# Kernel tuning notes

Hardware: AMD Instinct MI355X
Metric: run time of the kernel (lower is better)

## Reference

```python
import jax, jax.numpy as jnp
import numpy as np
import math

B, N, F_IN, F_OUT = 16, 2048, 256, 64


def setup_inputs() -> dict:
    key = jax.random.key(0)
    k1, k2, k3, k4 = jax.random.split(key, 4)
    x = jax.random.normal(k1, (B, N, F_IN), dtype=jnp.float32)
    adj = jax.random.randint(k2, (B, N, N), 0, 2, dtype=jnp.int32)
    stdv = 1.0 / math.sqrt(F_OUT)
    weight = jax.random.uniform(k3, (F_IN, F_OUT), dtype=jnp.float32, minval=-stdv, maxval=stdv)
    # weight2 stdv = 1/sqrt(1) = 1.0
    weight2 = jax.random.uniform(k4, (2 * F_OUT, 1), dtype=jnp.float32, minval=-1.0, maxval=1.0)
    return {"x": x, "adj": adj, "weight": weight, "weight2": weight2}


def reference(x, adj, weight, weight2):
    # h[b,n,o] = (x @ weight)  -- shared linear projection
    h = jnp.einsum("bni,io->bno", x, weight)
    Fo = weight.shape[1]
    # Split additive-attention vector: e_ij = relu(h_i . a_src + h_j . a_dst)
    # Mathematically identical to cat([h_i, h_j]) @ weight2 of the original.
    a_src = weight2[:Fo, 0]
    a_dst = weight2[Fo:, 0]
    s_src = jnp.einsum("bno,o->bn", h, a_src)  # [B, N]
    s_dst = jnp.einsum("bno,o->bn", h, a_dst)  # [B, N]
    e = jax.nn.relu(s_src[:, :, None] + s_dst[:, None, :])  # [B, N, N]
    NEG = jnp.float32(-9e15)
    scores = jnp.where(adj > 0, e, NEG)
    attention = jax.nn.softmax(scores, axis=2)  # softmax over neighbors j
    # dropout = 0.0 / eval mode -> identity
    out = jnp.einsum("bij,bjo->bio", attention, h)  # [B, N, F_OUT]
    return out
```

## Files before the change

### kernel.cpp

```cpp
#include <hip/hip_runtime.h>
#include <hip/hip_bf16.h>

#define BB 16
#define NN 2048
#define FIN 256
#define FO 64
#define CH 256
#define HSTR 264

typedef __bf16 bf16x8 __attribute__((ext_vector_type(8)));
typedef float  f32x4  __attribute__((ext_vector_type(4)));
typedef int    i32x4  __attribute__((ext_vector_type(4)));
typedef unsigned int uint;

__global__ __launch_bounds__(256) void k_pack(const int* __restrict__ adj,
                                              unsigned char* __restrict__ mask) {
    size_t t = (size_t)blockIdx.x * 256 + threadIdx.x;
    const i32x4* ap = (const i32x4*)(adj + t * 8);
    i32x4 a0 = __builtin_nontemporal_load(ap);
    i32x4 a1 = __builtin_nontemporal_load(ap + 1);
    unsigned b = (unsigned)(a0.x > 0) | ((unsigned)(a0.y > 0) << 1) |
                 ((unsigned)(a0.z > 0) << 2) | ((unsigned)(a0.w > 0) << 3) |
                 ((unsigned)(a1.x > 0) << 4) | ((unsigned)(a1.y > 0) << 5) |
                 ((unsigned)(a1.z > 0) << 6) | ((unsigned)(a1.w > 0) << 7);
    mask[t] = (unsigned char)b;
}

__global__ __launch_bounds__(256) void k1_gemm(
    const float* __restrict__ x, const float* __restrict__ weight,
    const float* __restrict__ w2,
    __bf16* __restrict__ hT, float* __restrict__ s_src, float* __restrict__ s_dst) {
    __shared__ __bf16 WtL[FO * 264];
    __shared__ float vsL[FIN], vdL[FIN];
    int t = threadIdx.x;
    {
        const float4* wr = (const float4*)(weight + t * FO);
        float a = 0.f, d = 0.f;
#pragma unroll
        for (int c = 0; c < 16; ++c) {
            float4 v = wr[c];
            int o = c * 4;
            WtL[(o + 0) * 264 + t] = (__bf16)v.x;
            WtL[(o + 1) * 264 + t] = (__bf16)v.y;
            WtL[(o + 2) * 264 + t] = (__bf16)v.z;
            WtL[(o + 3) * 264 + t] = (__bf16)v.w;
            a += v.x * w2[o] + v.y * w2[o + 1] + v.z * w2[o + 2] + v.w * w2[o + 3];
            d += v.x * w2[FO + o] + v.y * w2[FO + o + 1] +
                 v.z * w2[FO + o + 2] + v.w * w2[FO + o + 3];
        }
        vsL[t] = a;
        vdL[t] = d;
    }
    __syncthreads();

    int lane = threadIdx.x & 63, w = threadIdx.x >> 6;
    int quad = lane >> 4, m = lane & 15;
    int Rbase = blockIdx.x * 64 + w * 16;
    int R = Rbase + m;
    const float* xr = x + (long)R * FIN;

    f32x4 acc[4] = {};
    float ps = 0.f, pd = 0.f;

#pragma unroll
    for (int k0 = 0; k0 < FIN; k0 += 32) {
        int kb = k0 + quad * 8;
        float4 x0 = *(const float4*)(xr + kb);
        float4 x1 = *(const float4*)(xr + kb + 4);
        float4 u0 = *(const float4*)(vsL + kb);
        float4 u1 = *(const float4*)(vsL + kb + 4);
        float4 t0 = *(const float4*)(vdL + kb);
        float4 t1 = *(const float4*)(vdL + kb + 4);
        ps += x0.x * u0.x + x0.y * u0.y + x0.z * u0.z + x0.w * u0.w +
              x1.x * u1.x + x1.y * u1.y + x1.z * u1.z + x1.w * u1.w;
        pd += x0.x * t0.x + x0.y * t0.y + x0.z * t0.z + x0.w * t0.w +
              x1.x * t1.x + x1.y * t1.y + x1.z * t1.z + x1.w * t1.w;
        bf16x8 bf = {(__bf16)x0.x, (__bf16)x0.y, (__bf16)x0.z, (__bf16)x0.w,
                     (__bf16)x1.x, (__bf16)x1.y, (__bf16)x1.z, (__bf16)x1.w};
#pragma unroll
        for (int ot = 0; ot < 4; ++ot) {
            bf16x8 af = *(const bf16x8*)(WtL + (ot * 16 + m) * 264 + kb);
            acc[ot] = __builtin_amdgcn_mfma_f32_16x16x32_bf16(af, bf, acc[ot], 0, 0, 0);
        }
    }
    ps += __shfl_xor(ps, 16);
    ps += __shfl_xor(ps, 32);
    pd += __shfl_xor(pd, 16);
    pd += __shfl_xor(pd, 32);
    if (quad == 0) {
        s_src[R] = ps;
        s_dst[R] = pd;
    }
    int b = R >> 11;
    int nb = Rbase & (NN - 1);
#pragma unroll
    for (int ot = 0; ot < 4; ++ot) {
#pragma unroll
        for (int r = 0; r < 4; ++r) {
            int o = ot * 16 + quad * 4 + r;
            hT[((long)b * FO + o) * NN + nb + m] = (__bf16)acc[ot][r];
        }
    }
}

__global__ __launch_bounds__(256, 2) void k2_attn(
    const unsigned char* __restrict__ mask, const float* __restrict__ s_src,
    const float* __restrict__ s_dst, const __bf16* __restrict__ hT,
    float* __restrict__ out) {
    __shared__ __bf16 hL[FO * HSTR];
    __shared__ float EL[NN];
    int b = blockIdx.x >> 5;
    int i0 = (blockIdx.x & 31) << 6;
    int lane = threadIdx.x & 63, w = threadIdx.x >> 6;
    int quad = lane >> 4, m = lane & 15;
    int rowbase = i0 + w * 16;
    int row = rowbase + m;

    const float* sd = s_dst + b * NN;
    float mx = -3.0e38f;
    for (int j = lane; j < NN; j += 64) mx = fmaxf(mx, sd[j]);
#pragma unroll
    for (int off = 32; off >= 1; off >>= 1) mx = fmaxf(mx, __shfl_xor(mx, off));
    {
        int j0 = threadIdx.x * 8;
        float4 v0 = *(const float4*)(sd + j0);
        float4 v1 = *(const float4*)(sd + j0 + 4);
        EL[j0 + 0] = __expf(v0.x - mx);
        EL[j0 + 1] = __expf(v0.y - mx);
        EL[j0 + 2] = __expf(v0.z - mx);
        EL[j0 + 3] = __expf(v0.w - mx);
        EL[j0 + 4] = __expf(v1.x - mx);
        EL[j0 + 5] = __expf(v1.y - mx);
        EL[j0 + 6] = __expf(v1.z - mx);
        EL[j0 + 7] = __expf(v1.w - mx);
    }

    float T = s_src[b * NN + row] + mx;
    float cK = __expf(-T);

    int so = threadIdx.x >> 2;
    int sc = (threadIdx.x & 3) * 64;
    const __bf16* hsrc = hT + ((long)b * FO + so) * NN + sc;
    __bf16* hdst = hL + so * HSTR + sc;

    const uint4* mrow = (const uint4*)(mask + ((size_t)(b * NN + row)) * 256);
    int q8 = quad * 8;

    bf16x8 st[8];
    {
        const bf16x8* sp = (const bf16x8*)hsrc;
#pragma unroll
        for (int i = 0; i < 8; ++i) st[i] = sp[i];
    }
    uint4 mv0 = mrow[0], mv1 = mrow[1];

    f32x4 acc[4] = {};
    f32x4 accL = {};
    const bf16x8 ones = {(__bf16)1.f, (__bf16)1.f, (__bf16)1.f, (__bf16)1.f,
                         (__bf16)1.f, (__bf16)1.f, (__bf16)1.f, (__bf16)1.f};

    for (int c = 0; c < NN / CH; ++c) {
        __syncthreads();
        {
            bf16x8* dp = (bf16x8*)hdst;
#pragma unroll
            for (int i = 0; i < 8; ++i) dp[i] = st[i];
        }
        __syncthreads();
        uint mg[8] = {mv0.x, mv0.y, mv0.z, mv0.w, mv1.x, mv1.y, mv1.z, mv1.w};
        if (c < NN / CH - 1) {
            const bf16x8* sp = (const bf16x8*)(hsrc + (c + 1) * CH);
#pragma unroll
            for (int i = 0; i < 8; ++i) st[i] = sp[i];
            mv0 = mrow[(c + 1) * 2];
            mv1 = mrow[(c + 1) * 2 + 1];
        }
#pragma unroll
        for (int u = 0; u < 8; ++u) {
            int ksg = c * 8 + u;
            uint mb = (mg[u] >> q8) & 0xffu;
            const float* ep = EL + ksg * 32 + q8;
            float4 e0 = *(const float4*)ep;
            float4 e1 = *(const float4*)(ep + 4);
            float p0 = (mb & 1u)   ? fmaxf(e0.x, cK) : 0.f;
            float p1 = (mb & 2u)   ? fmaxf(e0.y, cK) : 0.f;
            float p2 = (mb & 4u)   ? fmaxf(e0.z, cK) : 0.f;
            float p3 = (mb & 8u)   ? fmaxf(e0.w, cK) : 0.f;
            float p4 = (mb & 16u)  ? fmaxf(e1.x, cK) : 0.f;
            float p5 = (mb & 32u)  ? fmaxf(e1.y, cK) : 0.f;
            float p6 = (mb & 64u)  ? fmaxf(e1.z, cK) : 0.f;
            float p7 = (mb & 128u) ? fmaxf(e1.w, cK) : 0.f;
            bf16x8 af = {(__bf16)p0, (__bf16)p1, (__bf16)p2, (__bf16)p3,
                         (__bf16)p4, (__bf16)p5, (__bf16)p6, (__bf16)p7};
            accL = __builtin_amdgcn_mfma_f32_16x16x32_bf16(af, ones, accL, 0, 0, 0);
            const __bf16* hb = hL + u * 32 + q8;
#pragma unroll
            for (int ot = 0; ot < 4; ++ot) {
                bf16x8 bf = *(const bf16x8*)(hb + (ot * 16 + m) * HSTR);
                acc[ot] = __builtin_amdgcn_mfma_f32_16x16x32_bf16(af, bf, acc[ot], 0, 0, 0);
            }
        }
    }

    float* outp = out + ((long)b * NN + rowbase) * FO;
#pragma unroll
    for (int r = 0; r < 4; ++r) {
        int orow = quad * 4 + r;
        float inv = 1.0f / accL[r];
#pragma unroll
        for (int ot = 0; ot < 4; ++ot) {
            outp[(long)orow * FO + ot * 16 + m] = acc[ot][r] * inv;
        }
    }
}

extern "C" void kernel_launch(void* const* d_in, const int* in_sizes, int n_in,
                              void* d_out, int out_size, void* d_ws, size_t ws_size,
                              hipStream_t stream) {
    const float* x      = (const float*)d_in[0];
    const int*   adj    = (const int*)d_in[1];
    const float* weight = (const float*)d_in[2];
    const float* w2     = (const float*)d_in[3];
    float* out = (float*)d_out;

    char* ws = (char*)d_ws;
    __bf16* hT   = (__bf16*)ws;
    float* s_src = (float*)(ws + 4194304);
    float* s_dst = (float*)(ws + 4194304 + 131072);
    unsigned char* mask = (unsigned char*)(ws + 4194304 + 262144);

    k_pack<<<32768, 256, 0, stream>>>(adj, mask);
    k1_gemm<<<512, 256, 0, stream>>>(x, weight, w2, hT, s_src, s_dst);
    k2_attn<<<512, 256, 0, stream>>>(mask, s_src, s_dst, hT, out);
}
```

Before: 408.0 us.

## Process two row tiles per wave and double-buffer h chunks in k2_attn

Each wave now computes 32 output rows instead of 16, sharing each shared-memory h fragment and EL load across two MFMA accumulator sets, and the grid halves to 256 blocks. The h staging buffer is double-buffered so only one barrier per chunk is needed. This is meant to cut shared-memory traffic, redundant per-block softmax preprocessing and sync overhead, at the cost of more registers, one block per CU and fewer total waves to hide latency.

```diff
diff --git a/kernel.cpp b/kernel.cpp
--- a/kernel.cpp
+++ b/kernel.cpp
@@ -103,18 +103,19 @@
     }
 }
 
-__global__ __launch_bounds__(256, 2) void k2_attn(
+__global__ __launch_bounds__(256, 1) void k2_attn(
     const unsigned char* __restrict__ mask, const float* __restrict__ s_src,
     const float* __restrict__ s_dst, const __bf16* __restrict__ hT,
     float* __restrict__ out) {
-    __shared__ __bf16 hL[FO * HSTR];
+    __shared__ __bf16 hL[2][FO * HSTR];
     __shared__ float EL[NN];
-    int b = blockIdx.x >> 5;
-    int i0 = (blockIdx.x & 31) << 6;
+    int b = blockIdx.x >> 4;
+    int i0 = (blockIdx.x & 15) << 7;
     int lane = threadIdx.x & 63, w = threadIdx.x >> 6;
     int quad = lane >> 4, m = lane & 15;
-    int rowbase = i0 + w * 16;
-    int row = rowbase + m;
+    int rowbase = i0 + w * 32;
+    int row0 = rowbase + m;
+    int row1 = rowbase + 16 + m;
 
     const float* sd = s_dst + b * NN;
     float mx = -3.0e38f;
@@ -135,15 +136,16 @@
         EL[j0 + 7] = __expf(v1.w - mx);
     }
 
-    float T = s_src[b * NN + row] + mx;
-    float cK = __expf(-T);
+    float cK0 = __expf(-(s_src[b * NN + row0] + mx));
+    float cK1 = __expf(-(s_src[b * NN + row1] + mx));
 
     int so = threadIdx.x >> 2;
     int sc = (threadIdx.x & 3) * 64;
     const __bf16* hsrc = hT + ((long)b * FO + so) * NN + sc;
-    __bf16* hdst = hL + so * HSTR + sc;
-
-    const uint4* mrow = (const uint4*)(mask + ((size_t)(b * NN + row)) * 256);
+    int ldoff = so * HSTR + sc;
+
+    const uint4* mrow0 = (const uint4*)(mask + ((size_t)(b * NN + row0)) * 256);
+    const uint4* mrow1 = (const uint4*)(mask + ((size_t)(b * NN + row1)) * 256);
     int q8 = quad * 8;
 
     bf16x8 st[8];
@@ -152,64 +154,89 @@
 #pragma unroll
         for (int i = 0; i < 8; ++i) st[i] = sp[i];
     }
-    uint4 mv0 = mrow[0], mv1 = mrow[1];
-
-    f32x4 acc[4] = {};
-    f32x4 accL = {};
+    uint4 ma0 = mrow0[0], ma1 = mrow0[1];
+    uint4 mb0 = mrow1[0], mb1 = mrow1[1];
+    {
+        bf16x8* dp = (bf16x8*)(hL[0] + ldoff);
+#pragma unroll
+        for (int i = 0; i < 8; ++i) dp[i] = st[i];
+    }
+    __syncthreads();
+
+    f32x4 acc0[4] = {}, acc1[4] = {};
+    f32x4 accL0 = {}, accL1 = {};
     const bf16x8 ones = {(__bf16)1.f, (__bf16)1.f, (__bf16)1.f, (__bf16)1.f,
                          (__bf16)1.f, (__bf16)1.f, (__bf16)1.f, (__bf16)1.f};
 
+#pragma unroll
     for (int c = 0; c < NN / CH; ++c) {
-        __syncthreads();
-        {
-            bf16x8* dp = (bf16x8*)hdst;
-#pragma unroll
-            for (int i = 0; i < 8; ++i) dp[i] = st[i];
-        }
-        __syncthreads();
-        uint mg[8] = {mv0.x, mv0.y, mv0.z, mv0.w, mv1.x, mv1.y, mv1.z, mv1.w};
+        const __bf16* cur = hL[c & 1];
+        uint mg0[8] = {ma0.x, ma0.y, ma0.z, ma0.w, ma1.x, ma1.y, ma1.z, ma1.w};
+        uint mg1[8] = {mb0.x, mb0.y, mb0.z, mb0.w, mb1.x, mb1.y, mb1.z, mb1.w};
         if (c < NN / CH - 1) {
             const bf16x8* sp = (const bf16x8*)(hsrc + (c + 1) * CH);
 #pragma unroll
             for (int i = 0; i < 8; ++i) st[i] = sp[i];
-            mv0 = mrow[(c + 1) * 2];
-            mv1 = mrow[(c + 1) * 2 + 1];
+            ma0 = mrow0[(c + 1) * 2];
+            ma1 = mrow0[(c + 1) * 2 + 1];
+            mb0 = mrow1[(c + 1) * 2];
+            mb1 = mrow1[(c + 1) * 2 + 1];
         }
 #pragma unroll
         for (int u = 0; u < 8; ++u) {
-            int ksg = c * 8 + u;
-            uint mb = (mg[u] >> q8) & 0xffu;
-            const float* ep = EL + ksg * 32 + q8;
+            uint mA = (mg0[u] >> q8) & 0xffu;
+            uint mB = (mg1[u] >> q8) & 0xffu;
+            const float* ep = EL + (c * 8 + u) * 32 + q8;
             float4 e0 = *(const float4*)ep;
             float4 e1 = *(const float4*)(ep + 4);
-            float p0 = (mb & 1u)   ? fmaxf(e0.x, cK) : 0.f;
-            float p1 = (mb & 2u)   ? fmaxf(e0.y, cK) : 0.f;
-            float p2 = (mb & 4u)   ? fmaxf(e0.z, cK) : 0.f;
-            float p3 = (mb & 8u)   ? fmaxf(e0.w, cK) : 0.f;
-            float p4 = (mb & 16u)  ? fmaxf(e1.x, cK) : 0.f;
-            float p5 = (mb & 32u)  ? fmaxf(e1.y, cK) : 0.f;
-            float p6 = (mb & 64u)  ? fmaxf(e1.z, cK) : 0.f;
-            float p7 = (mb & 128u) ? fmaxf(e1.w, cK) : 0.f;
-            bf16x8 af = {(__bf16)p0, (__bf16)p1, (__bf16)p2, (__bf16)p3,
-                         (__bf16)p4, (__bf16)p5, (__bf16)p6, (__bf16)p7};
-            accL = __builtin_amdgcn_mfma_f32_16x16x32_bf16(af, ones, accL, 0, 0, 0);
-            const __bf16* hb = hL + u * 32 + q8;
+            float a0 = (mA & 1u)   ? fmaxf(e0.x, cK0) : 0.f;
+            float a1 = (mA & 2u)   ? fmaxf(e0.y, cK0) : 0.f;
+            float a2 = (mA & 4u)   ? fmaxf(e0.z, cK0) : 0.f;
+            float a3 = (mA & 8u)   ? fmaxf(e0.w, cK0) : 0.f;
+            float a4 = (mA & 16u)  ? fmaxf(e1.x, cK0) : 0.f;
+            float a5 = (mA & 32u)  ? fmaxf(e1.y, cK0) : 0.f;
+            float a6 = (mA & 64u)  ? fmaxf(e1.z, cK0) : 0.f;
+            float a7 = (mA & 128u) ? fmaxf(e1.w, cK0) : 0.f;
+            float b0 = (mB & 1u)   ? fmaxf(e0.x, cK1) : 0.f;
+            float b1 = (mB & 2u)   ? fmaxf(e0.y, cK1) : 0.f;
+            float b2 = (mB & 4u)   ? fmaxf(e0.z, cK1) : 0.f;
+            float b3 = (mB & 8u)   ? fmaxf(e0.w, cK1) : 0.f;
+            float b4 = (mB & 16u)  ? fmaxf(e1.x, cK1) : 0.f;
+            float b5 = (mB & 32u)  ? fmaxf(e1.y, cK1) : 0.f;
+            float b6 = (mB & 64u)  ? fmaxf(e1.z, cK1) : 0.f;
+            float b7 = (mB & 128u) ? fmaxf(e1.w, cK1) : 0.f;
+            bf16x8 af0 = {(__bf16)a0, (__bf16)a1, (__bf16)a2, (__bf16)a3,
+                          (__bf16)a4, (__bf16)a5, (__bf16)a6, (__bf16)a7};
+            bf16x8 af1 = {(__bf16)b0, (__bf16)b1, (__bf16)b2, (__bf16)b3,
+                          (__bf16)b4, (__bf16)b5, (__bf16)b6, (__bf16)b7};
+            accL0 = __builtin_amdgcn_mfma_f32_16x16x32_bf16(af0, ones, accL0, 0, 0, 0);
+            accL1 = __builtin_amdgcn_mfma_f32_16x16x32_bf16(af1, ones, accL1, 0, 0, 0);
+            const __bf16* hb = cur + u * 32 + q8;
 #pragma unroll
             for (int ot = 0; ot < 4; ++ot) {
                 bf16x8 bf = *(const bf16x8*)(hb + (ot * 16 + m) * HSTR);
-                acc[ot] = __builtin_amdgcn_mfma_f32_16x16x32_bf16(af, bf, acc[ot], 0, 0, 0);
+                acc0[ot] = __builtin_amdgcn_mfma_f32_16x16x32_bf16(af0, bf, acc0[ot], 0, 0, 0);
+                acc1[ot] = __builtin_amdgcn_mfma_f32_16x16x32_bf16(af1, bf, acc1[ot], 0, 0, 0);
             }
         }
+        if (c < NN / CH - 1) {
+            bf16x8* dp = (bf16x8*)(hL[(c + 1) & 1] + ldoff);
+#pragma unroll
+            for (int i = 0; i < 8; ++i) dp[i] = st[i];
+        }
+        __syncthreads();
     }
 
     float* outp = out + ((long)b * NN + rowbase) * FO;
 #pragma unroll
     for (int r = 0; r < 4; ++r) {
-        int orow = quad * 4 + r;
-        float inv = 1.0f / accL[r];
+        int orow0 = quad * 4 + r;
+        float inv0 = 1.0f / accL0[r];
+        float inv1 = 1.0f / accL1[r];
 #pragma unroll
         for (int ot = 0; ot < 4; ++ot) {
-            outp[(long)orow * FO + ot * 16 + m] = acc[ot][r] * inv;
+            outp[(long)orow0 * FO + ot * 16 + m] = acc0[ot][r] * inv0;
+            outp[(long)(orow0 + 16) * FO + ot * 16 + m] = acc1[ot][r] * inv1;
         }
     }
 }
@@ -231,5 +258,5 @@
 
     k_pack<<<32768, 256, 0, stream>>>(adj, mask);
     k1_gemm<<<512, 256, 0, stream>>>(x, weight, w2, hT, s_src, s_dst);
-    k2_attn<<<512, 256, 0, stream>>>(mask, s_src, s_dst, hT, out);
-}
+    k2_attn<<<256, 256, 0, stream>>>(mask, s_src, s_dst, hT, out);
+}
```

Measured after the change: 404.3 us. No clear change (-0.9%).

## Fuse adjacency mask packing into attention kernel and double-buffer h tiles

Applied to the files above, without the earlier changes.

Drops the separate pack kernel that turned the int32 adjacency into a bitmask. The attention kernel now reads adj rows directly from global memory, prefetching the next chunk into registers. It also double-buffers the h tile in shared memory, so each chunk needs one barrier instead of two. This removes one full pass over adj plus a launch, but every attention block now streams the 4-byte-per-element adj itself and holds 16 extra vector registers, which may reduce occupancy.

```diff
diff --git a/kernel.cpp b/kernel.cpp
--- a/kernel.cpp
+++ b/kernel.cpp
@@ -12,19 +12,6 @@
 typedef float  f32x4  __attribute__((ext_vector_type(4)));
 typedef int    i32x4  __attribute__((ext_vector_type(4)));
 typedef unsigned int uint;
-
-__global__ __launch_bounds__(256) void k_pack(const int* __restrict__ adj,
-                                              unsigned char* __restrict__ mask) {
-    size_t t = (size_t)blockIdx.x * 256 + threadIdx.x;
-    const i32x4* ap = (const i32x4*)(adj + t * 8);
-    i32x4 a0 = __builtin_nontemporal_load(ap);
-    i32x4 a1 = __builtin_nontemporal_load(ap + 1);
-    unsigned b = (unsigned)(a0.x > 0) | ((unsigned)(a0.y > 0) << 1) |
-                 ((unsigned)(a0.z > 0) << 2) | ((unsigned)(a0.w > 0) << 3) |
-                 ((unsigned)(a1.x > 0) << 4) | ((unsigned)(a1.y > 0) << 5) |
-                 ((unsigned)(a1.z > 0) << 6) | ((unsigned)(a1.w > 0) << 7);
-    mask[t] = (unsigned char)b;
-}
 
 __global__ __launch_bounds__(256) void k1_gemm(
     const float* __restrict__ x, const float* __restrict__ weight,
@@ -104,10 +91,10 @@
 }
 
 __global__ __launch_bounds__(256, 2) void k2_attn(
-    const unsigned char* __restrict__ mask, const float* __restrict__ s_src,
+    const int* __restrict__ adj, const float* __restrict__ s_src,
     const float* __restrict__ s_dst, const __bf16* __restrict__ hT,
     float* __restrict__ out) {
-    __shared__ __bf16 hL[FO * HSTR];
+    __shared__ __bf16 hL[2][FO * HSTR];
     __shared__ float EL[NN];
     int b = blockIdx.x >> 5;
     int i0 = (blockIdx.x & 31) << 6;
@@ -135,24 +122,35 @@
         EL[j0 + 7] = __expf(v1.w - mx);
     }
 
-    float T = s_src[b * NN + row] + mx;
-    float cK = __expf(-T);
+    float cK = __expf(-(s_src[b * NN + row] + mx));
+
+    const i32x4* arow = (const i32x4*)(adj + ((size_t)(b * NN + row)) * NN);
+    int aq = quad * 2;
 
     int so = threadIdx.x >> 2;
     int sc = (threadIdx.x & 3) * 64;
     const __bf16* hsrc = hT + ((long)b * FO + so) * NN + sc;
-    __bf16* hdst = hL + so * HSTR + sc;
-
-    const uint4* mrow = (const uint4*)(mask + ((size_t)(b * NN + row)) * 256);
+    int ldoff = so * HSTR + sc;
     int q8 = quad * 8;
 
+    i32x4 A[16];
+#pragma unroll
+    for (int u = 0; u < 8; ++u) {
+        A[2 * u]     = arow[u * 8 + aq];
+        A[2 * u + 1] = arow[u * 8 + aq + 1];
+    }
     bf16x8 st[8];
     {
         const bf16x8* sp = (const bf16x8*)hsrc;
 #pragma unroll
         for (int i = 0; i < 8; ++i) st[i] = sp[i];
     }
-    uint4 mv0 = mrow[0], mv1 = mrow[1];
+    {
+        bf16x8* dp = (bf16x8*)(hL[0] + ldoff);
+#pragma unroll
+        for (int i = 0; i < 8; ++i) dp[i] = st[i];
+    }
+    __syncthreads();
 
     f32x4 acc[4] = {};
     f32x4 accL = {};
@@ -160,46 +158,52 @@
                          (__bf16)1.f, (__bf16)1.f, (__bf16)1.f, (__bf16)1.f};
 
     for (int c = 0; c < NN / CH; ++c) {
-        __syncthreads();
-        {
-            bf16x8* dp = (bf16x8*)hdst;
-#pragma unroll
-            for (int i = 0; i < 8; ++i) dp[i] = st[i];
-        }
-        __syncthreads();
-        uint mg[8] = {mv0.x, mv0.y, mv0.z, mv0.w, mv1.x, mv1.y, mv1.z, mv1.w};
-        if (c < NN / CH - 1) {
-            const bf16x8* sp = (const bf16x8*)(hsrc + (c + 1) * CH);
-#pragma unroll
-            for (int i = 0; i < 8; ++i) st[i] = sp[i];
-            mv0 = mrow[(c + 1) * 2];
-            mv1 = mrow[(c + 1) * 2 + 1];
-        }
+        const __bf16* cur = hL[c & 1];
+        bf16x8 af[8];
 #pragma unroll
         for (int u = 0; u < 8; ++u) {
-            int ksg = c * 8 + u;
-            uint mb = (mg[u] >> q8) & 0xffu;
-            const float* ep = EL + ksg * 32 + q8;
+            const float* ep = EL + (c * 8 + u) * 32 + q8;
             float4 e0 = *(const float4*)ep;
             float4 e1 = *(const float4*)(ep + 4);
-            float p0 = (mb & 1u)   ? fmaxf(e0.x, cK) : 0.f;
-            float p1 = (mb & 2u)   ? fmaxf(e0.y, cK) : 0.f;
-            float p2 = (mb & 4u)   ? fmaxf(e0.z, cK) : 0.f;
-            float p3 = (mb & 8u)   ? fmaxf(e0.w, cK) : 0.f;
-            float p4 = (mb & 16u)  ? fmaxf(e1.x, cK) : 0.f;
-            float p5 = (mb & 32u)  ? fmaxf(e1.y, cK) : 0.f;
-            float p6 = (mb & 64u)  ? fmaxf(e1.z, cK) : 0.f;
-            float p7 = (mb & 128u) ? fmaxf(e1.w, cK) : 0.f;
-            bf16x8 af = {(__bf16)p0, (__bf16)p1, (__bf16)p2, (__bf16)p3,
-                         (__bf16)p4, (__bf16)p5, (__bf16)p6, (__bf16)p7};
-            accL = __builtin_amdgcn_mfma_f32_16x16x32_bf16(af, ones, accL, 0, 0, 0);
-            const __bf16* hb = hL + u * 32 + q8;
+            i32x4 a0 = A[2 * u], a1 = A[2 * u + 1];
+            float p0 = (a0.x > 0) ? fmaxf(e0.x, cK) : 0.f;
+            float p1 = (a0.y > 0) ? fmaxf(e0.y, cK) : 0.f;
+            float p2 = (a0.z > 0) ? fmaxf(e0.z, cK) : 0.f;
+            float p3 = (a0.w > 0) ? fmaxf(e0.w, cK) : 0.f;
+            float p4 = (a1.x > 0) ? fmaxf(e1.x, cK) : 0.f;
+            float p5 = (a1.y > 0) ? fmaxf(e1.y, cK) : 0.f;
+            float p6 = (a1.z > 0) ? fmaxf(e1.z, cK) : 0.f;
+            float p7 = (a1.w > 0) ? fmaxf(e1.w, cK) : 0.f;
+            af[u] = bf16x8{(__bf16)p0, (__bf16)p1, (__bf16)p2, (__bf16)p3,
+                           (__bf16)p4, (__bf16)p5, (__bf16)p6, (__bf16)p7};
+        }
+        if (c < NN / CH - 1) {
+            const i32x4* an = arow + (c + 1) * 64;
+#pragma unroll
+            for (int u = 0; u < 8; ++u) {
+                A[2 * u]     = an[u * 8 + aq];
+                A[2 * u + 1] = an[u * 8 + aq + 1];
+            }
+            const bf16x8* sp = (const bf16x8*)(hsrc + (c + 1) * CH);
+#pragma unroll
+            for (int i = 0; i < 8; ++i) st[i] = sp[i];
+        }
+#pragma unroll
+        for (int u = 0; u < 8; ++u) {
+            accL = __builtin_amdgcn_mfma_f32_16x16x32_bf16(af[u], ones, accL, 0, 0, 0);
+            const __bf16* hb = cur + u * 32 + q8;
 #pragma unroll
             for (int ot = 0; ot < 4; ++ot) {
                 bf16x8 bf = *(const bf16x8*)(hb + (ot * 16 + m) * HSTR);
-                acc[ot] = __builtin_amdgcn_mfma_f32_16x16x32_bf16(af, bf, acc[ot], 0, 0, 0);
+                acc[ot] = __builtin_amdgcn_mfma_f32_16x16x32_bf16(af[u], bf, acc[ot], 0, 0, 0);
             }
         }
+        if (c < NN / CH - 1) {
+            bf16x8* dp = (bf16x8*)(hL[(c + 1) & 1] + ldoff);
+#pragma unroll
+            for (int i = 0; i < 8; ++i) dp[i] = st[i];
+        }
+        __syncthreads();
     }
 
     float* outp = out + ((long)b * NN + rowbase) * FO;
@@ -227,9 +231,7 @@
     __bf16* hT   = (__bf16*)ws;
     float* s_src = (float*)(ws + 4194304);
     float* s_dst = (float*)(ws + 4194304 + 131072);
-    unsigned char* mask = (unsigned char*)(ws + 4194304 + 262144);
-
-    k_pack<<<32768, 256, 0, stream>>>(adj, mask);
+
     k1_gemm<<<512, 256, 0, stream>>>(x, weight, w2, hT, s_src, s_dst);
-    k2_attn<<<512, 256, 0, stream>>>(mask, s_src, s_dst, hT, out);
+    k2_attn<<<512, 256, 0, stream>>>(adj, s_src, s_dst, hT, out);
 }
```

Measured after the change: 394.6 us. 3.3% less time.
